# Kernel tuning notes

Hardware: AMD Instinct MI355X
Metric: run time of the kernel (lower is better)

## Reference

```python
import jax, jax.numpy as jnp
import numpy as np

GROUPS = 8
HEADS = 4
EPS = 1e-5


def setup_inputs() -> dict:
    key = jax.random.key(0)
    ks = jax.random.split(key, 3)
    b, c, h, w = 4, 256, 64, 64
    x = jax.random.normal(ks[0], (b, c, h, w), dtype=jnp.float32)
    gn_gamma = jnp.ones((c,), jnp.float32)
    gn_beta = jnp.zeros((c,), jnp.float32)
    w_qkv = jax.random.normal(ks[1], (3 * c, c), dtype=jnp.float32) * (c ** -0.5)
    w_proj = jax.random.normal(ks[2], (c, c), dtype=jnp.float32) * (c ** -0.5)
    b_proj = jnp.zeros((c,), jnp.float32)
    return {"x": x, "gn_gamma": gn_gamma, "gn_beta": gn_beta,
            "w_qkv": w_qkv, "w_proj": w_proj, "b_proj": b_proj}


def reference(x, gn_gamma, gn_beta, w_qkv, w_proj, b_proj):
    b, c, h, w = x.shape
    residual = x
    # GroupNorm(8, c)
    xg = x.reshape(b, GROUPS, -1)
    mean = jnp.mean(xg, axis=-1, keepdims=True)
    var = jnp.var(xg, axis=-1, keepdims=True)
    xn = ((xg - mean) * jax.lax.rsqrt(var + EPS)).reshape(b, c, h, w)
    xn = xn * gn_gamma[:, None, None] + gn_beta[:, None, None]
    # QKV conv1x1 (no bias)
    qkv = jnp.einsum('oc,bchw->bohw', w_qkv, xn)  # [b,3c,h,w]
    q, k, v = jnp.split(qkv, 3, axis=1)
    n = h * w
    dh = c // HEADS
    q = q.reshape(b, HEADS, dh, n)
    k = k.reshape(b, HEADS, dh, n)
    v = v.reshape(b, HEADS, dh, n)
    scale = (c * HEADS) ** (-0.5)
    attn = jnp.einsum('bhci,bhcj->bhij', q, k) * scale  # [b,H,n,n]
    attn = jax.nn.softmax(attn, axis=-1)
    out = jnp.einsum('bhij,bhcj->bhci', attn, v).reshape(b, c, h, w)
    out = jnp.einsum('oc,bchw->bohw', w_proj, out) + b_proj[:, None, None]
    return out + residual
```

## Files before the change

kernel.cpp:

```cpp
#include <hip/hip_runtime.h>
#include <math.h>
#include <stdint.h>

#define B_ 4
#define C_ 256
#define HW_ 4096
#define G_ 8
#define H_ 4
#define DH_ 64
#define GRP_ELEMS (32 * HW_)
#define NCHUNK 16
#define CHUNK_ELEMS (GRP_ELEMS / NCHUNK)
#define EPS 1e-5f
#define NT_ (HW_ / 64)
#define QSCALE 0.04508422f

typedef __attribute__((ext_vector_type(8))) short short8;
typedef __attribute__((ext_vector_type(4))) float f32x4;
typedef __attribute__((ext_vector_type(4))) unsigned int u32x4;
typedef const __attribute__((address_space(1))) uint32_t* gas1_t;
typedef __attribute__((address_space(3))) uint32_t* las3_t;

__device__ __forceinline__ ushort f2bf(float x) {
    unsigned u = __builtin_bit_cast(unsigned, x);
    u += 0x7FFFu + ((u >> 16) & 1u);
    return (ushort)(u >> 16);
}
__device__ __forceinline__ uint32_t cvt_pk_bf16(float lo, float hi) {
    uint32_t r;
    asm("v_cvt_pk_bf16_f32 %0, %1, %2" : "=v"(r) : "v"(lo), "v"(hi));
    return r;
}

__global__ __launch_bounds__(256) void gn_partial(const float* __restrict__ x,
                                                  float* __restrict__ part) {
    int bg = blockIdx.x >> 4;
    int chunk = blockIdx.x & 15;
    const float4* p = (const float4*)(x + (size_t)bg * GRP_ELEMS + (size_t)chunk * CHUNK_ELEMS);
    int t = threadIdx.x;
    float s = 0.f, ss = 0.f;
#pragma unroll
    for (int i = 0; i < 8; ++i) {
        float4 v = p[t + i * 256];
        s  += v.x + v.y + v.z + v.w;
        ss += v.x * v.x + v.y * v.y + v.z * v.z + v.w * v.w;
    }
#pragma unroll
    for (int off = 32; off; off >>= 1) {
        s  += __shfl_xor(s, off, 64);
        ss += __shfl_xor(ss, off, 64);
    }
    __shared__ float ls[8];
    int wave = t >> 6, lane = t & 63;
    if (lane == 0) { ls[wave * 2] = s; ls[wave * 2 + 1] = ss; }
    __syncthreads();
    if (t == 0) {
        float S = 0.f, SS = 0.f;
#pragma unroll
        for (int w = 0; w < 4; ++w) { S += ls[w * 2]; SS += ls[w * 2 + 1]; }
        part[(bg * 16 + chunk) * 2]     = S;
        part[(bg * 16 + chunk) * 2 + 1] = SS;
    }
}

__global__ __launch_bounds__(256) void wcvt(const float* __restrict__ wq,
                                            const float* __restrict__ wp,
                                            ushort* __restrict__ wqb,
                                            ushort* __restrict__ wpb) {
    int i = blockIdx.x * 256 + threadIdx.x;
    if (i < 768 * 256) {
        float s = (i < 256 * 256) ? QSCALE : 1.0f;
        wqb[i] = f2bf(wq[i] * s);
    } else {
        int j = i - 768 * 256;
        wpb[j] = f2bf(wp[j]);
    }
}

#define TSTR 264
__global__ __launch_bounds__(256) void gn_qkv(const float* __restrict__ x,
                                              const float* __restrict__ gamma,
                                              const float* __restrict__ beta,
                                              const float* __restrict__ part,
                                              const ushort* __restrict__ wqb,
                                              ushort* __restrict__ qt,
                                              ushort* __restrict__ kt,
                                              ushort* __restrict__ vv) {
    __shared__ float2 affs[256];
    __shared__ __align__(16) ushort Ts[64 * TSTR];
    int n0 = blockIdx.x * 64;
    int b  = blockIdx.y;
    int t = threadIdx.x;

    {
        int c = t;
        int bg = b * G_ + (c >> 5);
        float S = 0.f, SS = 0.f;
#pragma unroll
        for (int i = 0; i < 16; ++i) {
            S  += part[(bg * 16 + i) * 2];
            SS += part[(bg * 16 + i) * 2 + 1];
        }
        float mean = S * (1.f / GRP_ELEMS);
        float var  = SS * (1.f / GRP_ELEMS) - mean * mean;
        float inv  = rsqrtf(var + EPS);
        float a = inv * gamma[c];
        affs[c] = make_float2(a, beta[c] - mean * a);
    }
    __syncthreads();

    {
        int n4 = t & 15, cr = t >> 4;
#pragma unroll
        for (int ct = 0; ct < 16; ++ct) {
            int c = cr + 16 * ct;
            float2 p = affs[c];
            float4 v = *(const float4*)(x + ((size_t)(b * C_ + c)) * HW_ + n0 + n4 * 4);
            ushort e[4];
            e[0] = f2bf(v.x * p.x + p.y); e[1] = f2bf(v.y * p.x + p.y);
            e[2] = f2bf(v.z * p.x + p.y); e[3] = f2bf(v.w * p.x + p.y);
#pragma unroll
            for (int k = 0; k < 4; ++k) {
                int n = n4 * 4 + k;
                Ts[n * TSTR + (((c >> 3) ^ ((n >> 2) & 7)) << 3) + (c & 7)] = e[k];
            }
        }
    }
    __syncthreads();

    int w = t >> 6, lane = t & 63, l16 = lane & 15, lg = lane >> 4;

    for (int z = 0; z < 3; ++z) {
        const ushort* wz = wqb + (size_t)(z * 256 + 32 * w + l16) * C_;
        f32x4 acc[2][2][4];
#pragma unroll
        for (int j = 0; j < 2; ++j)
#pragma unroll
            for (int os = 0; os < 2; ++os)
#pragma unroll
                for (int u = 0; u < 4; ++u)
#pragma unroll
                    for (int r = 0; r < 4; ++r) acc[j][os][u][r] = 0.f;

#pragma unroll 2
        for (int ks = 0; ks < 8; ++ks) {
            short8 a00 = *(const short8*)(wz + 32 * ks + 8 * lg);
            short8 a01 = *(const short8*)(wz + 16 * C_ + 32 * ks + 8 * lg);
            short8 a10 = *(const short8*)(wz + 128 * C_ + 32 * ks + 8 * lg);
            short8 a11 = *(const short8*)(wz + 144 * C_ + 32 * ks + 8 * lg);
#pragma unroll
            for (int u = 0; u < 4; ++u) {
                int n = 16 * u + l16;
                short8 bf = *(const short8*)&Ts[n * TSTR +
                               (((4 * ks + lg) ^ ((n >> 2) & 7)) << 3)];
                acc[0][0][u] = __builtin_amdgcn_mfma_f32_16x16x32_bf16(a00, bf, acc[0][0][u], 0, 0, 0);
                acc[0][1][u] = __builtin_amdgcn_mfma_f32_16x16x32_bf16(a01, bf, acc[0][1][u], 0, 0, 0);
                acc[1][0][u] = __builtin_amdgcn_mfma_f32_16x16x32_bf16(a10, bf, acc[1][0][u], 0, 0, 0);
                acc[1][1][u] = __builtin_amdgcn_mfma_f32_16x16x32_bf16(a11, bf, acc[1][1][u], 0, 0, 0);
            }
        }

#pragma unroll
        for (int j = 0; j < 2; ++j)
#pragma unroll
            for (int os = 0; os < 2; ++os) {
                int o_base = z * 256 + 128 * j + 32 * w + 16 * os;
                if (z < 2) {
                    int h = (o_base >> 6) & 3;
                    int od0 = (o_base & 63) + 4 * lg;
                    ushort* dstb = (z ? kt : qt) + ((size_t)((b << 2) | h) * HW_) * DH_;
#pragma unroll
                    for (int u = 0; u < 4; ++u) {
                        int n = n0 + 16 * u + l16;
                        uint2 pk;
                        pk.x = cvt_pk_bf16(acc[j][os][u][0], acc[j][os][u][1]);
                        pk.y = cvt_pk_bf16(acc[j][os][u][2], acc[j][os][u][3]);
                        *(uint2*)(dstb + (size_t)n * DH_ + od0) = pk;
                    }
                } else {
                    int row0 = o_base - 512 + 4 * lg;
#pragma unroll
                    for (int u = 0; u < 4; ++u) {
                        int n = n0 + 16 * u + l16;
#pragma unroll
                        for (int r = 0; r < 4; ++r)
                            vv[((size_t)(b * C_ + row0 + r)) * HW_ + n] = f2bf(acc[j][os][u][r]);
                    }
                }
            }
    }
}

__global__ __launch_bounds__(256) void flash_attn_mfma(const ushort* __restrict__ qt,
                                                       const ushort* __restrict__ kt,
                                                       const ushort* __restrict__ vv,
                                                       ushort* __restrict__ attT) {
    __shared__ __align__(16) ushort Kb[4][64 * 64];
    __shared__ __align__(16) ushort Vb[4][64 * 64];

    int bid = blockIdx.x;
    int wg = (bid & 7) * 64 + (bid >> 3);
    int bh = wg >> 5;
    int i0 = (wg & 31) * 128;
    int b = bh >> 2, h = bh & 3;
    int t = threadIdx.x;
    int w = t >> 6, lane = t & 63, l16 = lane & 15, lg = lane >> 4;
    const ushort* qtb = qt + (size_t)bh * HW_ * DH_;
    const ushort* ktb = kt + (size_t)bh * HW_ * DH_;
    const ushort* vb  = vv + ((size_t)(b * C_) + h * DH_) * HW_;

    short8 qf[2][2];
#pragma unroll
    for (int s = 0; s < 2; ++s)
#pragma unroll
        for (int ks = 0; ks < 2; ++ks)
            qf[s][ks] = *(const short8*)(qtb + (size_t)(i0 + 32 * w + 16 * s + l16) * DH_ + 32 * ks + 8 * lg);

    f32x4 O0[4], O1[4], lacc0, lacc1;
#pragma unroll
    for (int dt = 0; dt < 4; ++dt)
#pragma unroll
        for (int r = 0; r < 4; ++r) { O0[dt][r] = 0.f; O1[dt][r] = 0.f; }
#pragma unroll
    for (int r = 0; r < 4; ++r) { lacc0[r] = 0.f; lacc1[r] = 0.f; }
    const f32x4 Z4 = {0.f, 0.f, 0.f, 0.f};

    u32x4 ov; ov[0] = ov[1] = ov[2] = ov[3] = 0x3F803F80u;
    short8 onesf = __builtin_bit_cast(short8, ov);

    int r8 = lane >> 3, ch8 = lane & 7;
    size_t koff[2], voff[2];
#pragma unroll
    for (int half = 0; half < 2; ++half) {
        int L = 16 * w + half * 8 + r8;
        int gk = (L & 0x23) | ((L & 0x0C) << 1) | ((L & 0x10) >> 2);
        koff[half] = (size_t)gk * DH_ + ((ch8 ^ (L & 7)) << 3);
        voff[half] = (size_t)L * HW_ + ((ch8 ^ (L & 7)) << 3);
    }

    auto stageK = [&](int bi, int j0) {
#pragma unroll
        for (int half = 0; half < 2; ++half) {
            int rowb = 16 * w + half * 8;
            __builtin_amdgcn_global_load_lds((gas1_t)(ktb + (size_t)j0 * DH_ + koff[half]),
                (las3_t)&Kb[bi][rowb * 64], 16, 0, 0);
        }
    };
    auto stageV = [&](int bi, int j0) {
#pragma unroll
        for (int half = 0; half < 2; ++half) {
            int rowb = 16 * w + half * 8;
            __builtin_amdgcn_global_load_lds((gas1_t)(vb + (size_t)j0 + voff[half]),
                (las3_t)&Vb[bi][rowb * 64], 16, 0, 0);
        }
    };

    auto qk2 = [&](int bi, f32x4* S0, f32x4* S1) {
        __builtin_amdgcn_s_setprio(1);
#pragma unroll
        for (int jt = 0; jt < 4; ++jt) {
            short8 kf0 = *(const short8*)&Kb[bi][(16 * jt + l16) * 64 +
                                                ((lg ^ (l16 & 7)) << 3)];
            S0[jt] = __builtin_amdgcn_mfma_f32_16x16x32_bf16(kf0, qf[0][0], Z4, 0, 0, 0);
            S1[jt] = __builtin_amdgcn_mfma_f32_16x16x32_bf16(kf0, qf[1][0], Z4, 0, 0, 0);
            short8 kf1 = *(const short8*)&Kb[bi][(16 * jt + l16) * 64 +
                                                (((4 + lg) ^ (l16 & 7)) << 3)];
            S0[jt] = __builtin_amdgcn_mfma_f32_16x16x32_bf16(kf1, qf[0][1], S0[jt], 0, 0, 0);
            S1[jt] = __builtin_amdgcn_mfma_f32_16x16x32_bf16(kf1, qf[1][1], S1[jt], 0, 0, 0);
        }
        __builtin_amdgcn_s_setprio(0);
    };

    auto pv2 = [&](int bi, short8* pf0, short8* pf1) {
        __builtin_amdgcn_s_setprio(1);
#pragma unroll
        for (int dt = 0; dt < 4; ++dt) {
#pragma unroll
            for (int ks = 0; ks < 2; ++ks) {
                short8 vf = *(const short8*)&Vb[bi][(16 * dt + l16) * 64 +
                                                    (((4 * ks + lg) ^ (l16 & 7)) << 3)];
                O0[dt] = __builtin_amdgcn_mfma_f32_16x16x32_bf16(vf, pf0[ks], O0[dt], 0, 0, 0);
                O1[dt] = __builtin_amdgcn_mfma_f32_16x16x32_bf16(vf, pf1[ks], O1[dt], 0, 0, 0);
            }
        }
        lacc0 = __builtin_amdgcn_mfma_f32_16x16x32_bf16(onesf, pf0[0], lacc0, 0, 0, 0);
        lacc0 = __builtin_amdgcn_mfma_f32_16x16x32_bf16(onesf, pf0[1], lacc0, 0, 0, 0);
        lacc1 = __builtin_amdgcn_mfma_f32_16x16x32_bf16(onesf, pf1[0], lacc1, 0, 0, 0);
        lacc1 = __builtin_amdgcn_mfma_f32_16x16x32_bf16(onesf, pf1[1], lacc1, 0, 0, 0);
        __builtin_amdgcn_s_setprio(0);
    };

    auto softmax_pf = [&](f32x4* S, short8* pf) {
#pragma unroll
        for (int jt = 0; jt < 4; ++jt)
#pragma unroll
            for (int r = 0; r < 4; ++r)
                S[jt][r] = __builtin_amdgcn_exp2f(S[jt][r]);
#pragma unroll
        for (int ks = 0; ks < 2; ++ks) {
            u32x4 p;
            p[0] = cvt_pk_bf16(S[2 * ks][0],     S[2 * ks][1]);
            p[1] = cvt_pk_bf16(S[2 * ks][2],     S[2 * ks][3]);
            p[2] = cvt_pk_bf16(S[2 * ks + 1][0], S[2 * ks + 1][1]);
            p[3] = cvt_pk_bf16(S[2 * ks + 1][2], S[2 * ks + 1][3]);
            pf[ks] = __builtin_bit_cast(short8, p);
        }
    };

    f32x4 Sa0[4], Sa1[4], Sb0[4], Sb1[4];

    auto body = [&](int VW, int KR, int KW, int VR,
                    f32x4* SC0, f32x4* SC1, f32x4* SN0, f32x4* SN1,
                    int tt, int drain) {
        if (tt + 2 < NT_) stageV(VW, (tt + 2) * 64);
        qk2(KR, SN0, SN1);
        if (tt + 3 < NT_) stageK(KW, (tt + 3) * 64);
        short8 pf0[2], pf1[2];
        softmax_pf(SC0, pf0);
        softmax_pf(SC1, pf1);
        pv2(VR, pf0, pf1);
        if (drain == 8)      asm volatile("s_waitcnt vmcnt(8)" ::: "memory");
        else if (drain == 4) asm volatile("s_waitcnt vmcnt(4)" ::: "memory");
        else                 asm volatile("s_waitcnt vmcnt(0)" ::: "memory");
        __builtin_amdgcn_s_barrier();
    };

    stageK(0, 0); stageV(0, 0);
    stageK(1, 64); stageV(1, 64);
    stageK(2, 128);
    asm volatile("s_waitcnt vmcnt(0)" ::: "memory");
    __builtin_amdgcn_s_barrier();
    qk2(0, Sa0, Sa1);

    for (int g = 0; g < 15; ++g) {
        body(2, 1, 3, 0, Sa0, Sa1, Sb0, Sb1, 4 * g + 0, 8);
        body(3, 2, 0, 1, Sb0, Sb1, Sa0, Sa1, 4 * g + 1, 8);
        body(0, 3, 1, 2, Sa0, Sa1, Sb0, Sb1, 4 * g + 2, 8);
        body(1, 0, 2, 3, Sb0, Sb1, Sa0, Sa1, 4 * g + 3, 8);
    }
    body(2, 1, 3, 0, Sa0, Sa1, Sb0, Sb1, 60, 8);
    body(3, 2, 0, 1, Sb0, Sb1, Sa0, Sa1, 61, 4);
    body(0, 3, 1, 2, Sa0, Sa1, Sb0, Sb1, 62, 0);
    {
        short8 pf0[2], pf1[2];
        softmax_pf(Sb0, pf0);
        softmax_pf(Sb1, pf1);
        pv2(3, pf0, pf1);
    }

    float inv0 = 1.f / lacc0[0], inv1 = 1.f / lacc1[0];
    ushort* ab0 = attT + ((size_t)b * HW_ + i0 + 32 * w + l16) * C_ + h * DH_;
    ushort* ab1 = ab0 + 16 * C_;
#pragma unroll
    for (int dt = 0; dt < 4; ++dt) {
        uint2 p0, p1;
        p0.x = cvt_pk_bf16(O0[dt][0] * inv0, O0[dt][1] * inv0);
        p0.y = cvt_pk_bf16(O0[dt][2] * inv0, O0[dt][3] * inv0);
        *(uint2*)(ab0 + 16 * dt + 4 * lg) = p0;
        p1.x = cvt_pk_bf16(O1[dt][0] * inv1, O1[dt][1] * inv1);
        p1.y = cvt_pk_bf16(O1[dt][2] * inv1, O1[dt][3] * inv1);
        *(uint2*)(ab1 + 16 * dt + 4 * lg) = p1;
    }
}

__global__ __launch_bounds__(256) void proj_gemm(const ushort* __restrict__ wpb,
                                                 const ushort* __restrict__ attT,
                                                 const float* __restrict__ bias,
                                                 const float* __restrict__ x,
                                                 float* __restrict__ out) {
    int n0 = blockIdx.x * 64;
    int o0 = blockIdx.y * 128;
    int b  = blockIdx.z;
    int t = threadIdx.x;
    int w = t >> 6, lane = t & 63, l16 = lane & 15, lg = lane >> 4;
    const ushort* xb = attT + ((size_t)b * HW_ + n0) * C_;
    const ushort* wrow0 = wpb + (size_t)(o0 + 32 * w + l16) * C_;
    const ushort* wrow1 = wrow0 + 16 * C_;

    f32x4 acc[2][4];
#pragma unroll
    for (int os = 0; os < 2; ++os)
#pragma unroll
        for (int u = 0; u < 4; ++u)
#pragma unroll
            for (int r = 0; r < 4; ++r) acc[os][u][r] = 0.f;

#pragma unroll 2
    for (int ks = 0; ks < 8; ++ks) {
        short8 a0 = *(const short8*)(wrow0 + 32 * ks + 8 * lg);
        short8 a1 = *(const short8*)(wrow1 + 32 * ks + 8 * lg);
#pragma unroll
        for (int u = 0; u < 4; ++u) {
            short8 bf = *(const short8*)(xb + (size_t)(16 * u + l16) * C_ + 32 * ks + 8 * lg);
            acc[0][u] = __builtin_amdgcn_mfma_f32_16x16x32_bf16(a0, bf, acc[0][u], 0, 0, 0);
            acc[1][u] = __builtin_amdgcn_mfma_f32_16x16x32_bf16(a1, bf, acc[1][u], 0, 0, 0);
        }
    }

#pragma unroll
    for (int os = 0; os < 2; ++os) {
        int o_base = o0 + 32 * w + 16 * os;
#pragma unroll
        for (int u = 0; u < 4; ++u) {
            int n = n0 + 16 * u + l16;
#pragma unroll
            for (int r = 0; r < 4; ++r) {
                int mrow = o_base + 4 * lg + r;
                size_t idx = ((size_t)(b * C_ + mrow)) * HW_ + n;
                out[idx] = acc[os][u][r] + bias[mrow] + x[idx];
            }
        }
    }
}

extern "C" void kernel_launch(void* const* d_in, const int* in_sizes, int n_in,
                              void* d_out, int out_size, void* d_ws, size_t ws_size,
                              hipStream_t stream) {
    const float* x        = (const float*)d_in[0];
    const float* gn_gamma = (const float*)d_in[1];
    const float* gn_beta  = (const float*)d_in[2];
    const float* w_qkv    = (const float*)d_in[3];
    const float* w_proj   = (const float*)d_in[4];
    const float* b_proj   = (const float*)d_in[5];
    float* out = (float*)d_out;

    ushort* wsp  = (ushort*)d_ws;
    ushort* qt   = wsp;
    ushort* kt   = qt   + 4194304;
    ushort* vv   = kt   + 4194304;
    ushort* attT = vv   + 4194304;
    ushort* wqb  = attT + 4194304;
    ushort* wpb  = wqb  + 196608;
    float*  part = (float*)(wpb + 65536);

    gn_partial<<<dim3(G_ * B_ * NCHUNK), 256, 0, stream>>>(x, part);
    wcvt<<<dim3(1024), 256, 0, stream>>>(w_qkv, w_proj, wqb, wpb);
    gn_qkv<<<dim3(HW_ / 64, B_), 256, 0, stream>>>(x, gn_gamma, gn_beta, part, wqb, qt, kt, vv);
    flash_attn_mfma<<<dim3(512), 256, 0, stream>>>(qt, kt, vv, attT);
    proj_gemm<<<dim3(HW_ / 64, 2, B_), 256, 0, stream>>>(wpb, attT, b_proj, x, out);
}
```

Before: 122.2 us.

## Load V fragments directly into registers and fuse GN stats with weight conversion

```diff
diff --git a/kernel.cpp b/kernel.cpp
--- a/kernel.cpp
+++ b/kernel.cpp
@@ -32,12 +32,26 @@
     return r;
 }
 
-__global__ __launch_bounds__(256) void gn_partial(const float* __restrict__ x,
-                                                  float* __restrict__ part) {
+__global__ __launch_bounds__(256) void gn_part_wcvt(const float* __restrict__ x,
+                                                    float* __restrict__ part,
+                                                    const float* __restrict__ wq,
+                                                    const float* __restrict__ wp,
+                                                    ushort* __restrict__ wqb,
+                                                    ushort* __restrict__ wpb) {
+    int t = threadIdx.x;
+    if (blockIdx.x >= 512) {
+        int i = (blockIdx.x - 512) * 256 + t;
+        if (i < 768 * 256) {
+            float s = (i < 256 * 256) ? QSCALE : 1.0f;
+            wqb[i] = f2bf(wq[i] * s);
+        } else {
+            wpb[i - 768 * 256] = f2bf(wp[i - 768 * 256]);
+        }
+        return;
+    }
     int bg = blockIdx.x >> 4;
     int chunk = blockIdx.x & 15;
     const float4* p = (const float4*)(x + (size_t)bg * GRP_ELEMS + (size_t)chunk * CHUNK_ELEMS);
-    int t = threadIdx.x;
     float s = 0.f, ss = 0.f;
 #pragma unroll
     for (int i = 0; i < 8; ++i) {
@@ -60,20 +74,6 @@
         for (int w = 0; w < 4; ++w) { S += ls[w * 2]; SS += ls[w * 2 + 1]; }
         part[(bg * 16 + chunk) * 2]     = S;
         part[(bg * 16 + chunk) * 2 + 1] = SS;
-    }
-}
-
-__global__ __launch_bounds__(256) void wcvt(const float* __restrict__ wq,
-                                            const float* __restrict__ wp,
-                                            ushort* __restrict__ wqb,
-                                            ushort* __restrict__ wpb) {
-    int i = blockIdx.x * 256 + threadIdx.x;
-    if (i < 768 * 256) {
-        float s = (i < 256 * 256) ? QSCALE : 1.0f;
-        wqb[i] = f2bf(wq[i] * s);
-    } else {
-        int j = i - 768 * 256;
-        wpb[j] = f2bf(wp[j]);
     }
 }
 
@@ -196,7 +196,6 @@
                                                        const ushort* __restrict__ vv,
                                                        ushort* __restrict__ attT) {
     __shared__ __align__(16) ushort Kb[4][64 * 64];
-    __shared__ __align__(16) ushort Vb[4][64 * 64];
 
     int bid = blockIdx.x;
     int wg = (bid & 7) * 64 + (bid >> 3);
@@ -229,13 +228,12 @@
     short8 onesf = __builtin_bit_cast(short8, ov);
 
     int r8 = lane >> 3, ch8 = lane & 7;
-    size_t koff[2], voff[2];
+    size_t koff[2];
 #pragma unroll
     for (int half = 0; half < 2; ++half) {
         int L = 16 * w + half * 8 + r8;
         int gk = (L & 0x23) | ((L & 0x0C) << 1) | ((L & 0x10) >> 2);
         koff[half] = (size_t)gk * DH_ + ((ch8 ^ (L & 7)) << 3);
-        voff[half] = (size_t)L * HW_ + ((ch8 ^ (L & 7)) << 3);
     }
 
     auto stageK = [&](int bi, int j0) {
@@ -246,13 +244,12 @@
                 (las3_t)&Kb[bi][rowb * 64], 16, 0, 0);
         }
     };
-    auto stageV = [&](int bi, int j0) {
-#pragma unroll
-        for (int half = 0; half < 2; ++half) {
-            int rowb = 16 * w + half * 8;
-            __builtin_amdgcn_global_load_lds((gas1_t)(vb + (size_t)j0 + voff[half]),
-                (las3_t)&Vb[bi][rowb * 64], 16, 0, 0);
-        }
+    auto loadV = [&](short8 (*V)[2], int j0) {
+#pragma unroll
+        for (int dt = 0; dt < 4; ++dt)
+#pragma unroll
+            for (int ks = 0; ks < 2; ++ks)
+                V[dt][ks] = *(const short8*)(vb + (size_t)(16 * dt + l16) * HW_ + j0 + 32 * ks + 8 * lg);
     };
 
     auto qk2 = [&](int bi, f32x4* S0, f32x4* S1) {
@@ -271,16 +268,14 @@
         __builtin_amdgcn_s_setprio(0);
     };
 
-    auto pv2 = [&](int bi, short8* pf0, short8* pf1) {
+    auto pv2 = [&](short8 (*V)[2], short8* pf0, short8* pf1) {
         __builtin_amdgcn_s_setprio(1);
 #pragma unroll
         for (int dt = 0; dt < 4; ++dt) {
 #pragma unroll
             for (int ks = 0; ks < 2; ++ks) {
-                short8 vf = *(const short8*)&Vb[bi][(16 * dt + l16) * 64 +
-                                                    (((4 * ks + lg) ^ (l16 & 7)) << 3)];
-                O0[dt] = __builtin_amdgcn_mfma_f32_16x16x32_bf16(vf, pf0[ks], O0[dt], 0, 0, 0);
-                O1[dt] = __builtin_amdgcn_mfma_f32_16x16x32_bf16(vf, pf1[ks], O1[dt], 0, 0, 0);
+                O0[dt] = __builtin_amdgcn_mfma_f32_16x16x32_bf16(V[dt][ks], pf0[ks], O0[dt], 0, 0, 0);
+                O1[dt] = __builtin_amdgcn_mfma_f32_16x16x32_bf16(V[dt][ks], pf1[ks], O1[dt], 0, 0, 0);
             }
         }
         lacc0 = __builtin_amdgcn_mfma_f32_16x16x32_bf16(onesf, pf0[0], lacc0, 0, 0, 0);
@@ -308,44 +303,43 @@
     };
 
     f32x4 Sa0[4], Sa1[4], Sb0[4], Sb1[4];
-
-    auto body = [&](int VW, int KR, int KW, int VR,
-                    f32x4* SC0, f32x4* SC1, f32x4* SN0, f32x4* SN1,
-                    int tt, int drain) {
-        if (tt + 2 < NT_) stageV(VW, (tt + 2) * 64);
+    short8 vfA[4][2], vfB[4][2];
+
+    auto body = [&](int KR, int KW, f32x4* SC0, f32x4* SC1,
+                    f32x4* SN0, f32x4* SN1,
+                    short8 (*VA)[2], short8 (*VB)[2], int tt, int drain) {
         qk2(KR, SN0, SN1);
+        loadV(VB, (tt + 1) * 64);
         if (tt + 3 < NT_) stageK(KW, (tt + 3) * 64);
         short8 pf0[2], pf1[2];
         softmax_pf(SC0, pf0);
         softmax_pf(SC1, pf1);
-        pv2(VR, pf0, pf1);
-        if (drain == 8)      asm volatile("s_waitcnt vmcnt(8)" ::: "memory");
-        else if (drain == 4) asm volatile("s_waitcnt vmcnt(4)" ::: "memory");
-        else                 asm volatile("s_waitcnt vmcnt(0)" ::: "memory");
+        pv2(VA, pf0, pf1);
+        if (drain == 10)     asm volatile("s_waitcnt vmcnt(10)" ::: "memory");
+        else                 asm volatile("s_waitcnt vmcnt(8)" ::: "memory");
         __builtin_amdgcn_s_barrier();
     };
 
-    stageK(0, 0); stageV(0, 0);
-    stageK(1, 64); stageV(1, 64);
-    stageK(2, 128);
+    stageK(0, 0); stageK(1, 64); stageK(2, 128);
     asm volatile("s_waitcnt vmcnt(0)" ::: "memory");
     __builtin_amdgcn_s_barrier();
     qk2(0, Sa0, Sa1);
+    loadV(vfA, 0);
 
     for (int g = 0; g < 15; ++g) {
-        body(2, 1, 3, 0, Sa0, Sa1, Sb0, Sb1, 4 * g + 0, 8);
-        body(3, 2, 0, 1, Sb0, Sb1, Sa0, Sa1, 4 * g + 1, 8);
-        body(0, 3, 1, 2, Sa0, Sa1, Sb0, Sb1, 4 * g + 2, 8);
-        body(1, 0, 2, 3, Sb0, Sb1, Sa0, Sa1, 4 * g + 3, 8);
-    }
-    body(2, 1, 3, 0, Sa0, Sa1, Sb0, Sb1, 60, 8);
-    body(3, 2, 0, 1, Sb0, Sb1, Sa0, Sa1, 61, 4);
-    body(0, 3, 1, 2, Sa0, Sa1, Sb0, Sb1, 62, 0);
+        body(1, 3, Sa0, Sa1, Sb0, Sb1, vfA, vfB, 4 * g + 0, 10);
+        body(2, 0, Sb0, Sb1, Sa0, Sa1, vfB, vfA, 4 * g + 1, 10);
+        body(3, 1, Sa0, Sa1, Sb0, Sb1, vfA, vfB, 4 * g + 2, 10);
+        body(0, 2, Sb0, Sb1, Sa0, Sa1, vfB, vfA, 4 * g + 3, 10);
+    }
+    body(1, 3, Sa0, Sa1, Sb0, Sb1, vfA, vfB, 60, 10);
+    body(2, 0, Sb0, Sb1, Sa0, Sa1, vfB, vfA, 61, 8);
+    body(3, 1, Sa0, Sa1, Sb0, Sb1, vfA, vfB, 62, 8);
     {
         short8 pf0[2], pf1[2];
         softmax_pf(Sb0, pf0);
         softmax_pf(Sb1, pf1);
-        pv2(3, pf0, pf1);
+        pv2(vfB, pf0, pf1);
     }
 
     float inv0 = 1.f / lacc0[0], inv1 = 1.f / lacc1[0];
@@ -433,8 +427,7 @@
     ushort* wpb  = wqb  + 196608;
     float*  part = (float*)(wpb + 65536);
 
-    gn_partial<<<dim3(G_ * B_ * NCHUNK), 256, 0, stream>>>(x, part);
-    wcvt<<<dim3(1024), 256, 0, stream>>>(w_qkv, w_proj, wqb, wpb);
+    gn_part_wcvt<<<dim3(512 + 1024), 256, 0, stream>>>(x, part, w_qkv, w_proj, wqb, wpb);
     gn_qkv<<<dim3(HW_ / 64, B_), 256, 0, stream>>>(x, gn_gamma, gn_beta, part, wqb, qt, kt, vv);
     flash_attn_mfma<<<dim3(512), 256, 0, stream>>>(qt, kt, vv, attT);
     proj_gemm<<<dim3(HW_ / 64, 2, B_), 256, 0, stream>>>(wpb, attT, b_proj, x, out);
```

Result: slower. 211.7 us (+73.2%).
